# Optimization experiments

Measured on AMD Instinct MI355X. Metric: run time of the kernel, lower is better.

Reference implementation:

```python
import jax, jax.numpy as jnp
import numpy as np

HEADS = 16
PHI = (1.0 + np.sqrt(5.0)) / 2.0


def setup_inputs() -> dict:
    key = jax.random.key(0)
    k1, k2, k3, k4 = jax.random.split(key, 4)
    B, L, D = 2, 2048, 1024
    x = jax.random.normal(k1, (B, L, D), dtype=jnp.float32)
    # nn.Linear(dim, 3*dim, bias=False): store as [D, 3D] for x @ W
    w_qkv = jax.random.normal(k2, (D, 3 * D), dtype=jnp.float32) * (D ** -0.5)
    w_proj = jax.random.normal(k3, (D, D), dtype=jnp.float32) * (D ** -0.5)
    b_proj = jax.random.normal(k4, (D,), dtype=jnp.float32) * 0.01
    return {"x": x, "w_qkv": w_qkv, "w_proj": w_proj, "b_proj": b_proj}


def phi_bias(L):
    # pos[i] = (i * phi) mod 1 ; bias = log(exp(-|pos_i - pos_j|) + 1e-8)
    pos = (jnp.arange(L, dtype=jnp.float32) * PHI) % 1.0
    dist = jnp.abs(pos[:, None] - pos[None, :])  # [L, L]
    return jnp.log(jnp.exp(-dist) + 1e-8)


def reference(x, w_qkv, w_proj, b_proj):
    B, L, D = x.shape
    H = HEADS
    Dh = D // H
    scale = Dh ** -0.5
    qkv = (x @ w_qkv).reshape(B, L, 3, H, Dh)
    q = jnp.transpose(qkv[:, :, 0], (0, 2, 1, 3))  # [B, H, L, Dh]
    k = jnp.transpose(qkv[:, :, 1], (0, 2, 1, 3))
    v = jnp.transpose(qkv[:, :, 2], (0, 2, 1, 3))
    attn = jnp.einsum("bhid,bhjd->bhij", q, k) * scale  # [B, H, L, L]
    attn = attn + phi_bias(L)[None, None]  # additive phi-distance bias
    attn = jax.nn.softmax(attn, axis=-1)
    out = jnp.einsum("bhij,bhjd->bhid", attn, v)  # [B, H, L, Dh]
    out = jnp.transpose(out, (0, 2, 1, 3)).reshape(B, L, D)
    return out @ w_proj + b_proj
```

## Files before the change

kernel.cpp:

```cpp
#include <hip/hip_runtime.h>
#include <math.h>


typedef _Float16 f16;
typedef _Float16 f16x4 __attribute__((ext_vector_type(4)));
typedef _Float16 f16x8 __attribute__((ext_vector_type(8)));
typedef float f32x4 __attribute__((ext_vector_type(4)));

#define MFMA32(a, b, c) __builtin_amdgcn_mfma_f32_16x16x32_f16(a, b, c, 0, 0, 0)

static constexpr int Bsz = 2, Lseq = 2048, Dm = 1024, H = 16, Dh = 64;
static constexpr int Mtot = Bsz * Lseq;
static constexpr int NQKV = 3 * Dm;
static constexpr float PHI_F = 1.61803398874989484820f;
static constexpr float LOG2E = 1.44269504088896f;
static constexpr float QS = 0.125f * LOG2E;
static constexpr float CSTEP = 0.55417527999932633f;

__device__ __forceinline__ void load16_to_lds(const f16* g, f16* l) {
  __builtin_amdgcn_global_load_lds(
      (const __attribute__((address_space(1))) unsigned int*)g,
      (__attribute__((address_space(3))) unsigned int*)l, 16, 0, 0);
}

__device__ __forceinline__ void barrier_fenced() {
  __builtin_amdgcn_sched_barrier(0);
  __builtin_amdgcn_s_barrier();
  __builtin_amdgcn_sched_barrier(0);
}

__global__ __launch_bounds__(256) void prep_fused(
    const float* __restrict__ x, f16* __restrict__ xb,
    const float* __restrict__ wqkv, f16* __restrict__ wqkvT,
    const float* __restrict__ wproj, f16* __restrict__ wpT) {
  __shared__ float tile[32][33];
  int blk = blockIdx.x;
  if (blk < 4096) {
    int i = (blk * 256 + threadIdx.x) * 4;
    float4 v = *reinterpret_cast<const float4*>(x + i);
    f16 t[4] = {(f16)v.x, (f16)v.y, (f16)v.z, (f16)v.w};
    *reinterpret_cast<uint2*>(xb + i) = *reinterpret_cast<uint2*>(t);
    return;
  }
  const float* in;
  f16* out;
  int N, bx, by;
  if (blk < 7168) {
    int local = blk - 4096;
    bx = local % 96; by = local / 96; N = NQKV;
    in = wqkv; out = wqkvT;
  } else {
    int local = blk - 7168;
    bx = local & 31; by = local >> 5; N = Dm;
    in = wproj; out = wpT;
  }
  int n0 = bx * 32, k0 = by * 32;
  int tx = threadIdx.x & 31, ty = threadIdx.x >> 5;
#pragma unroll
  for (int r = 0; r < 32; r += 8)
    tile[ty + r][tx] = in[(size_t)(k0 + ty + r) * N + n0 + tx];
  __syncthreads();
#pragma unroll
  for (int r = 0; r < 32; r += 8)
    out[(size_t)(n0 + ty + r) * Dm + k0 + tx] = (f16)tile[tx][ty + r];
}

__global__ __launch_bounds__(512, 1) void gemm_qkv(
    const f16* __restrict__ A, const f16* __restrict__ Bt,
    f16* __restrict__ qb, f16* __restrict__ kb, f16* __restrict__ vb) {
  __shared__ f16 As[2 * 256 * 64];
  __shared__ f16 Bs[2 * 192 * 64];

  int tid = threadIdx.x;
  int wave = tid >> 6, lane = tid & 63;
  int quad = lane >> 4, l16 = lane & 15;
  int warp_m = wave >> 2, warp_n = wave & 3;
  int wm = warp_m * 128, wn = warp_n * 48;

  int lid = blockIdx.x;
  int xcd = lid & 7, t = lid >> 3;
  int mg = xcd & 3, ng = xcd >> 2;
  int m0 = (mg * 4 + (t >> 3)) * 256;
  int n0 = (ng * 8 + (t & 7)) * 192;

  const int gu = (lane & 7) ^ (lane >> 3);
  const f16* gAb = A + (size_t)(m0 + wave * 8 + (lane >> 3)) * Dm + gu * 8;
  const f16* gBb = Bt + (size_t)(n0 + wave * 8 + (lane >> 3)) * Dm + gu * 8;

  auto stageA = [&](int buf, int h, int kn) __attribute__((always_inline)) {
#pragma unroll
    for (int i = 0; i < 2; i++)
      load16_to_lds(gAb + (size_t)(h * 128 + i * 64) * Dm + kn,
                    As + buf * 16384 + (h * 128 + i * 64 + wave * 8) * 64);
  };
  auto stageB = [&](int buf, int part, int kn) __attribute__((always_inline)) {
    if (part == 0) {
#pragma unroll
      for (int i = 0; i < 2; i++)
        load16_to_lds(gBb + (size_t)(i * 64) * Dm + kn,
                      Bs + buf * 12288 + (i * 64 + wave * 8) * 64);
    } else {
      load16_to_lds(gBb + (size_t)128 * Dm + kn,
                    Bs + buf * 12288 + (128 + wave * 8) * 64);
    }
  };

  f32x4 acc[8][3] = {};

  auto do_tile = [&](int buf, int t_) __attribute__((always_inline)) {
    const f16* Ab = As + buf * 16384 + (wm + l16) * 64;
    const f16* Bb = Bs + buf * 12288 + (wn + l16) * 64;
    int nbuf = buf ^ 1;
    int kA = ((t_ + 1) & 15) * 64;
    int kB = ((t_ + 2) & 15) * 64;

    f16x8 a[4][2], b0[2][2], b1[2];

#pragma unroll
    for (int m = 0; m < 4; m++)
#pragma unroll
      for (int s = 0; s < 2; s++)
        a[m][s] = *reinterpret_cast<const f16x8*>(
            Ab + m * 16 * 64 + (((s * 4 + quad) ^ (l16 & 7)) * 8));
#pragma unroll
    for (int n = 0; n < 2; n++)
#pragma unroll
      for (int s = 0; s < 2; s++)
        b0[n][s] = *reinterpret_cast<const f16x8*>(
            Bb + n * 16 * 64 + (((s * 4 + quad) ^ (l16 & 7)) * 8));
    stageA(nbuf, 0, kA);
    barrier_fenced();
    asm volatile("s_waitcnt lgkmcnt(0)" ::: "memory");
    __builtin_amdgcn_sched_barrier(0);
    __builtin_amdgcn_s_setprio(1);
#pragma unroll
    for (int m = 0; m < 4; m++)
#pragma unroll
      for (int n = 0; n < 2; n++) {
        acc[m][n] = MFMA32(a[m][0], b0[n][0], acc[m][n]);
        acc[m][n] = MFMA32(a[m][1], b0[n][1], acc[m][n]);
      }
    __builtin_amdgcn_s_setprio(0);
    barrier_fenced();

#pragma unroll
    for (int s = 0; s < 2; s++)
      b1[s] = *reinterpret_cast<const f16x8*>(
          Bb + 2 * 16 * 64 + (((s * 4 + quad) ^ (l16 & 7)) * 8));
    stageA(nbuf, 1, kA);
    barrier_fenced();
    asm volatile("s_waitcnt lgkmcnt(0)" ::: "memory");
    __builtin_amdgcn_sched_barrier(0);
    __builtin_amdgcn_s_setprio(1);
#pragma unroll
    for (int m = 0; m < 4; m++) {
      acc[m][2] = MFMA32(a[m][0], b1[0], acc[m][2]);
      acc[m][2] = MFMA32(a[m][1], b1[1], acc[m][2]);
    }
    __builtin_amdgcn_s_setprio(0);
    barrier_fenced();

#pragma unroll
    for (int m = 0; m < 4; m++)
#pragma unroll
      for (int s = 0; s < 2; s++)
        a[m][s] = *reinterpret_cast<const f16x8*>(
            Ab + (4 + m) * 16 * 64 + (((s * 4 + quad) ^ (l16 & 7)) * 8));
    stageB(buf, 0, kB);
    barrier_fenced();
    asm volatile("s_waitcnt lgkmcnt(0)" ::: "memory");
    __builtin_amdgcn_sched_barrier(0);
    __builtin_amdgcn_s_setprio(1);
#pragma unroll
    for (int m = 0; m < 4; m++)
#pragma unroll
      for (int n = 0; n < 2; n++) {
        acc[4 + m][n] = MFMA32(a[m][0], b0[n][0], acc[4 + m][n]);
        acc[4 + m][n] = MFMA32(a[m][1], b0[n][1], acc[4 + m][n]);
      }
    __builtin_amdgcn_s_setprio(0);
    barrier_fenced();

    stageB(buf, 1, kB);
    asm volatile("s_waitcnt vmcnt(3)" ::: "memory");
    barrier_fenced();
    __builtin_amdgcn_s_setprio(1);
#pragma unroll
    for (int m = 0; m < 4; m++) {
      acc[4 + m][2] = MFMA32(a[m][0], b1[0], acc[4 + m][2]);
      acc[4 + m][2] = MFMA32(a[m][1], b1[1], acc[4 + m][2]);
    }
    __builtin_amdgcn_s_setprio(0);
    barrier_fenced();
  };

  stageA(0, 0, 0);
  stageA(0, 1, 0);
  stageB(0, 0, 0);
  stageB(0, 1, 0);
  stageB(1, 0, 64);
  stageB(1, 1, 64);
  asm volatile("s_waitcnt vmcnt(3)" ::: "memory");
  barrier_fenced();

#pragma unroll 1
  for (int tt = 0; tt < 16; tt += 2) {
    do_tile(0, tt);
    do_tile(1, tt + 1);
  }
  asm volatile("s_waitcnt vmcnt(0)" ::: "memory");

#pragma unroll
  for (int i = 0; i < 8; i++) {
#pragma unroll
    for (int j = 0; j < 3; j++) {
      int n = n0 + wn + j * 16 + l16;
      int ty = n >> 10;
      int df = n & 1023;
      int h = df >> 6, dh = df & 63;
      int mb = m0 + wm + i * 16 + quad * 4;
      int b = mb >> 11, l = mb & 2047;
      int bhh = b * H + h;
      if (ty == 2) {
        int jj = l & 63;
        int jh = jj >> 5, rem = jj & 31;
        int qd = (rem & 15) >> 2;
        int e0 = (rem >= 16) ? 4 : 0;
        f16x4 tmp;
#pragma unroll
        for (int r = 0; r < 4; r++) tmp[r] = (f16)acc[i][j][r];
        *reinterpret_cast<uint2*>(
            vb + (size_t)bhh * (Dh * Lseq) + (l >> 6) * 4096 + dh * 64 +
            (jh * 4 + qd) * 8 + e0) = *reinterpret_cast<uint2*>(&tmp);
      } else {
        size_t idx = (((size_t)bhh) * Lseq + l) * Dh + dh;
        if (ty == 0) {
#pragma unroll
          for (int r = 0; r < 4; r++)
            qb[idx + (size_t)r * Dh] = (f16)(acc[i][j][r] * QS);
        } else {
#pragma unroll
          for (int r = 0; r < 4; r++)
            kb[idx + (size_t)r * Dh] = (f16)acc[i][j][r];
        }
      }
    }
  }
}

__global__ __launch_bounds__(256) void gemm_proj(
    const f16* __restrict__ A, const f16* __restrict__ Bt,
    float* __restrict__ out, const float* __restrict__ bias) {
  constexpr int MI = 4, AI = 4;
  __shared__ f16 As[128 * 64];
  __shared__ f16 Bs[128 * 64];

  int tid = threadIdx.x;
  int wave = tid >> 6, lane = tid & 63;
  int quad = lane >> 4, l16 = lane & 15;
  int wm = (wave >> 1) * 64, wn = (wave & 1) * 64;

  int lid = blockIdx.x;
  int xcd = lid & 7, t = lid >> 3;
  int m0 = (xcd * 4 + (t >> 3)) * 128;
  int n0 = (t & 7) * 128;

  const int gu = (lane & 7) ^ (lane >> 3);
  const f16* gA[AI];
  f16* lA[AI];
#pragma unroll
  for (int i = 0; i < AI; i++) {
    int it = wave * AI + i;
    gA[i] = A + (size_t)(m0 + it * 8 + (lane >> 3)) * Dm + gu * 8;
    lA[i] = As + it * 512;
  }
  const f16* gB[4];
  f16* lB[4];
#pragma unroll
  for (int i = 0; i < 4; i++) {
    int it = wave * 4 + i;
    gB[i] = Bt + (size_t)(n0 + it * 8 + (lane >> 3)) * Dm + gu * 8;
    lB[i] = Bs + it * 512;
  }

  f32x4 acc[MI][4] = {};

  for (int k0 = 0; k0 < Dm; k0 += 64) {
#pragma unroll
    for (int i = 0; i < AI; i++) load16_to_lds(gA[i] + k0, lA[i]);
#pragma unroll
    for (int i = 0; i < 4; i++) load16_to_lds(gB[i] + k0, lB[i]);
    __syncthreads();
#pragma unroll
    for (int s = 0; s < 2; s++) {
      f16x8 a[MI], b[4];
#pragma unroll
      for (int i = 0; i < MI; i++) {
        int row = wm + i * 16 + l16;
        a[i] = *reinterpret_cast<const f16x8*>(
            As + row * 64 + (((s * 4 + quad) ^ (l16 & 7)) * 8));
      }
#pragma unroll
      for (int j = 0; j < 4; j++) {
        int row = wn + j * 16 + l16;
        b[j] = *reinterpret_cast<const f16x8*>(
            Bs + row * 64 + (((s * 4 + quad) ^ (l16 & 7)) * 8));
      }
#pragma unroll
      for (int i = 0; i < MI; i++)
#pragma unroll
        for (int j = 0; j < 4; j++)
          acc[i][j] = MFMA32(a[i], b[j], acc[i][j]);
    }
    __syncthreads();
  }

#pragma unroll
  for (int i = 0; i < MI; i++)
#pragma unroll
    for (int j = 0; j < 4; j++) {
      int n = n0 + wn + j * 16 + l16;
#pragma unroll
      for (int r = 0; r < 4; r++) {
        int m = m0 + wm + i * 16 + quad * 4 + r;
        out[(size_t)m * Dm + n] = acc[i][j][r] + bias[n];
      }
    }
}

__global__ __launch_bounds__(512, 4) void attn_kernel(
    const f16* __restrict__ qb,
    const f16* __restrict__ kb,
    const f16* __restrict__ vb,
    f16* __restrict__ ctx) {
  __shared__ __align__(16) unsigned char smem[33280];
  f16* Ks = (f16*)smem;
  f16* Vs = (f16*)(smem + 8192);

  int id = blockIdx.x;
  int bh = (id & 7) * 4 + ((id >> 3) >> 4);
  int q0 = ((id >> 3) & 15) * 128;

  int tid = threadIdx.x, wave = tid >> 6, lane = tid & 63;
  int quad = lane >> 4, l16 = lane & 15;
  int jhalf = wave >> 2, qq = wave & 3;

  f16x8 qfrag[2][2];
  float pq[2];
#pragma unroll
  for (int set = 0; set < 2; set++) {
    int q = q0 + qq * 32 + set * 16 + l16;
    const f16* Qrow = qb + ((size_t)bh * Lseq + q) * Dh;
    qfrag[set][0] = *reinterpret_cast<const f16x8*>(Qrow + quad * 8);
    qfrag[set][1] = *reinterpret_cast<const f16x8*>(Qrow + 32 + quad * 8);
    pq[set] = fmodf((float)q * PHI_F, 1.0f);
  }

  float pk[2][4];
#pragma unroll
  for (int jb = 0; jb < 2; jb++)
#pragma unroll
    for (int r = 0; r < 4; r++) {
      int j = jhalf * 32 + jb * 16 + quad * 4 + r;
      pk[jb][r] = fmodf((float)j * PHI_F, 1.0f);
    }

  const f16* Kbh = kb + (size_t)bh * Lseq * Dh;
  const f16* Vbh = vb + (size_t)bh * Dh * Lseq;
  const int gu = (lane & 7) ^ (lane >> 3);
  int g8 = wave * 8 + (lane >> 3);
  const f16* gK = Kbh + (size_t)g8 * Dh + gu * 8;
  const f16* gV = Vbh + (size_t)g8 * 64 + gu * 8;
  f16* lK = Ks + wave * 512;
  f16* lV = Vs + wave * 512;

  const f16 one = (f16)1.0f;
  const f16x8 ones8 = {one, one, one, one, one, one, one, one};

  f32x4 acc_o[2][4] = {};
  f32x4 acc_l[2] = {};

  for (int j0 = 0; j0 < Lseq; j0 += 64) {
    __syncthreads();
    load16_to_lds(gK + (size_t)j0 * Dh, lK);
    load16_to_lds(gV + (size_t)j0 * 64, lV);
    __syncthreads();

    f32x4 accs[2][2] = {};
#pragma unroll
    for (int s = 0; s < 2; s++)
#pragma unroll
      for (int jb = 0; jb < 2; jb++) {
        f16x8 kf = *reinterpret_cast<const f16x8*>(
            Ks + (jhalf * 32 + jb * 16 + l16) * 64 + (((s * 4 + quad) ^ (l16 & 7)) * 8));
        accs[0][jb] = MFMA32(kf, qfrag[0][s], accs[0][jb]);
        accs[1][jb] = MFMA32(kf, qfrag[1][s], accs[1][jb]);
      }

    f16x8 pf8[2];
#pragma unroll
    for (int set = 0; set < 2; set++) {
#pragma unroll
      for (int jb = 0; jb < 2; jb++) {
        float p[4];
#pragma unroll
        for (int r = 0; r < 4; r++) {
          float d = pq[set] - pk[jb][r];
          float arg = fmaf(-LOG2E, fabsf(d), accs[set][jb][r]);
          p[r] = __builtin_amdgcn_exp2f(arg);
        }
        auto lo = __builtin_amdgcn_cvt_pkrtz(p[0], p[1]);
        auto hi = __builtin_amdgcn_cvt_pkrtz(p[2], p[3]);
        pf8[set][jb * 4 + 0] = lo[0];
        pf8[set][jb * 4 + 1] = lo[1];
        pf8[set][jb * 4 + 2] = hi[0];
        pf8[set][jb * 4 + 3] = hi[1];
      }
      acc_l[set] = MFMA32(ones8, pf8[set], acc_l[set]);
    }
#pragma unroll
    for (int jb = 0; jb < 2; jb++)
#pragma unroll
      for (int r = 0; r < 4; r++)
        pk[jb][r] = __builtin_amdgcn_fractf(pk[jb][r] + CSTEP);

#pragma unroll
    for (int dblk = 0; dblk < 4; dblk++) {
      int row = dblk * 16 + l16;
      f16x8 va = *reinterpret_cast<const f16x8*>(
          Vs + row * 64 + (((jhalf * 4 + quad) ^ (l16 & 7)) * 8));
      acc_o[0][dblk] = MFMA32(va, pf8[0], acc_o[0][dblk]);
      acc_o[1][dblk] = MFMA32(va, pf8[1], acc_o[1][dblk]);
    }
  }

  __syncthreads();
  float* Oex = (float*)smem;
  float* Lex = (float*)(smem + 32768);
  if (jhalf == 1) {
#pragma unroll
    for (int set = 0; set < 2; set++) {
#pragma unroll
      for (int dblk = 0; dblk < 4; dblk++)
#pragma unroll
        for (int r = 0; r < 4; r++)
          Oex[(((qq * 2 + set) * 4 + dblk) * 16 + quad * 4 + r) * 16 + l16] =
              acc_o[set][dblk][r];
      if (quad == 0) Lex[(qq * 2 + set) * 16 + l16] = acc_l[set][0];
    }
  }
  __syncthreads();
  if (jhalf == 0) {
    int b = bh >> 4, h = bh & 15;
#pragma unroll
    for (int set = 0; set < 2; set++) {
      float ltot = acc_l[set][0] + Lex[(qq * 2 + set) * 16 + l16];
      float inv = 1.0f / ltot;
      int q = q0 + qq * 32 + set * 16 + l16;
      f16* crow = ctx + (size_t)(b * Lseq + q) * Dm + h * 64;
#pragma unroll
      for (int dblk = 0; dblk < 4; dblk++) {
        f16x4 o;
#pragma unroll
        for (int r = 0; r < 4; r++) {
          float full = acc_o[set][dblk][r] +
              Oex[(((qq * 2 + set) * 4 + dblk) * 16 + quad * 4 + r) * 16 + l16];
          o[r] = (f16)(full * inv);
        }
        *reinterpret_cast<uint2*>(crow + dblk * 16 + quad * 4) =
            *reinterpret_cast<uint2*>(&o);
      }
    }
  }
}

extern "C" void kernel_launch(void* const* d_in, const int* in_sizes, int n_in,
                              void* d_out, int out_size, void* d_ws, size_t ws_size,
                              hipStream_t stream) {
  const float* x      = (const float*)d_in[0];
  const float* w_qkv  = (const float*)d_in[1];
  const float* w_proj = (const float*)d_in[2];
  const float* b_proj = (const float*)d_in[3];
  float* out = (float*)d_out;

  f16* xb    = (f16*)d_ws;
  f16* wqkvT = xb + (size_t)Mtot * Dm;
  f16* wpT   = wqkvT + (size_t)NQKV * Dm;
  f16* qb    = wpT + (size_t)Dm * Dm;
  f16* kb    = qb + (size_t)Bsz * H * Lseq * Dh;
  f16* vb    = kb + (size_t)Bsz * H * Lseq * Dh;
  f16* ctx   = vb + (size_t)Bsz * H * Lseq * Dh;

  prep_fused<<<8192, 256, 0, stream>>>(x, xb, w_qkv, wqkvT, w_proj, wpT);

  gemm_qkv<<<256, 512, 0, stream>>>(xb, wqkvT, qb, kb, vb);

  attn_kernel<<<512, 512, 0, stream>>>(qb, kb, vb, ctx);

  gemm_proj<<<256, 256, 0, stream>>>(ctx, wpT, out, b_proj);
}
```

Measured before the change: 179.7 us.

## Double-buffer projection GEMM LDS tiles and raise wave priority around MFMA blocks

The output projection GEMM now uses two LDS buffers. Each iteration reads its fragments into registers, then issues the global-to-LDS load for the next K tile before running the MFMAs, so memory traffic overlaps with compute and one barrier per iteration is removed. The attention kernel and the GEMM also wrap their MFMA sequences in s_setprio(1)/s_setprio(0) to favour waves issuing matrix instructions. The GEMM's LDS footprint doubles, which may lower occupancy, and the fragment registers held per wave increase. The last iteration issues a wasted reload of tile 0.

```diff
diff --git a/kernel.cpp b/kernel.cpp
--- a/kernel.cpp
+++ b/kernel.cpp
@@ -252,8 +252,8 @@
     const f16* __restrict__ A, const f16* __restrict__ Bt,
     float* __restrict__ out, const float* __restrict__ bias) {
   constexpr int MI = 4, AI = 4;
-  __shared__ f16 As[128 * 64];
-  __shared__ f16 Bs[128 * 64];
+  __shared__ f16 As[2 * 128 * 64];
+  __shared__ f16 Bs[2 * 128 * 64];
 
   int tid = threadIdx.x;
   int wave = tid >> 6, lane = tid & 63;
@@ -283,36 +283,57 @@
     lB[i] = Bs + it * 512;
   }
 
+  auto stage = [&](int buf, int k0) __attribute__((always_inline)) {
+#pragma unroll
+    for (int i = 0; i < AI; i++) load16_to_lds(gA[i] + k0, lA[i] + buf * 8192);
+#pragma unroll
+    for (int i = 0; i < 4; i++) load16_to_lds(gB[i] + k0, lB[i] + buf * 8192);
+  };
+
   f32x4 acc[MI][4] = {};
 
-  for (int k0 = 0; k0 < Dm; k0 += 64) {
-#pragma unroll
-    for (int i = 0; i < AI; i++) load16_to_lds(gA[i] + k0, lA[i]);
-#pragma unroll
-    for (int i = 0; i < 4; i++) load16_to_lds(gB[i] + k0, lB[i]);
-    __syncthreads();
+  stage(0, 0);
+  asm volatile("s_waitcnt vmcnt(0)" ::: "memory");
+  barrier_fenced();
+
+#pragma unroll 1
+  for (int kt = 0; kt < 16; kt++) {
+    int buf = kt & 1;
+    const f16* Ab = As + buf * 8192;
+    const f16* Bb = Bs + buf * 8192;
+
+    f16x8 a[2][MI], b[2][4];
 #pragma unroll
     for (int s = 0; s < 2; s++) {
-      f16x8 a[MI], b[4];
 #pragma unroll
       for (int i = 0; i < MI; i++) {
         int row = wm + i * 16 + l16;
-        a[i] = *reinterpret_cast<const f16x8*>(
-            As + row * 64 + (((s * 4 + quad) ^ (l16 & 7)) * 8));
+        a[s][i] = *reinterpret_cast<const f16x8*>(
+            Ab + row * 64 + (((s * 4 + quad) ^ (l16 & 7)) * 8));
       }
 #pragma unroll
       for (int j = 0; j < 4; j++) {
         int row = wn + j * 16 + l16;
-        b[j] = *reinterpret_cast<const f16x8*>(
-            Bs + row * 64 + (((s * 4 + quad) ^ (l16 & 7)) * 8));
-      }
+        b[s][j] = *reinterpret_cast<const f16x8*>(
+            Bb + row * 64 + (((s * 4 + quad) ^ (l16 & 7)) * 8));
+      }
+    }
+
+    int kn = (kt + 1 < 16) ? (kt + 1) * 64 : 0;
+    stage(buf ^ 1, kn);
+
+    __builtin_amdgcn_s_setprio(1);
+#pragma unroll
+    for (int s = 0; s < 2; s++)
 #pragma unroll
       for (int i = 0; i < MI; i++)
 #pragma unroll
         for (int j = 0; j < 4; j++)
-          acc[i][j] = MFMA32(a[i], b[j], acc[i][j]);
-    }
-    __syncthreads();
+          acc[i][j] = MFMA32(a[s][i], b[s][j], acc[i][j]);
+    __builtin_amdgcn_s_setprio(0);
+
+    asm volatile("s_waitcnt vmcnt(0)" ::: "memory");
+    barrier_fenced();
   }
 
 #pragma unroll
@@ -387,6 +408,7 @@
     __syncthreads();
 
     f32x4 accs[2][2] = {};
+    __builtin_amdgcn_s_setprio(1);
 #pragma unroll
     for (int s = 0; s < 2; s++)
 #pragma unroll
@@ -396,6 +418,7 @@
         accs[0][jb] = MFMA32(kf, qfrag[0][s], accs[0][jb]);
         accs[1][jb] = MFMA32(kf, qfrag[1][s], accs[1][jb]);
       }
+    __builtin_amdgcn_s_setprio(0);
 
     f16x8 pf8[2];
 #pragma unroll
@@ -424,6 +447,7 @@
       for (int r = 0; r < 4; r++)
         pk[jb][r] = __builtin_amdgcn_fractf(pk[jb][r] + CSTEP);
 
+    __builtin_amdgcn_s_setprio(1);
 #pragma unroll
     for (int dblk = 0; dblk < 4; dblk++) {
       int row = dblk * 16 + l16;
@@ -432,6 +456,7 @@
       acc_o[0][dblk] = MFMA32(va, pf8[0], acc_o[0][dblk]);
       acc_o[1][dblk] = MFMA32(va, pf8[1], acc_o[1][dblk]);
     }
+    __builtin_amdgcn_s_setprio(0);
   }
 
   __syncthreads();
```

Measured after the change: 173.0 us. 1.04x faster.
